# Kernel tuning notes

Hardware: AMD Instinct MI355X
Metric: run time of the kernel (lower is better)

Reference implementation:

```python
import jax, jax.numpy as jnp
import numpy as np

B, N, D, H, FF = 2, 2048, 768, 12, 3072
HD = D // H
RADIUS = 2.0
COORD_DIM = 3
LN_EPS = 1e-5


def _layernorm(x, g, b):
    m = jnp.mean(x, axis=-1, keepdims=True)
    v = jnp.mean((x - m) ** 2, axis=-1, keepdims=True)
    return (x - m) * jax.lax.rsqrt(v + LN_EPS) * g + b


def setup_inputs() -> dict:
    key = jax.random.key(0)
    ks = jax.random.split(key, 16)
    s = 0.02
    return {
        "x": jax.random.normal(ks[0], (B, N, D), jnp.float32),
        "coords": jax.random.uniform(ks[1], (B, N, COORD_DIM), jnp.float32) * 10.0,
        "w_qkv": jax.random.normal(ks[2], (D, 3 * D), jnp.float32) * s,
        "b_qkv": jnp.zeros((3 * D,), jnp.float32),
        "w_out": jax.random.normal(ks[3], (D, D), jnp.float32) * s,
        "b_out": jnp.zeros((D,), jnp.float32),
        "w_ff1": jax.random.normal(ks[4], (D, FF), jnp.float32) * s,
        "b_ff1": jnp.zeros((FF,), jnp.float32),
        "w_ff2": jax.random.normal(ks[5], (FF, D), jnp.float32) * s,
        "b_ff2": jnp.zeros((D,), jnp.float32),
        "g1": jnp.ones((D,), jnp.float32),
        "beta1": jnp.zeros((D,), jnp.float32),
        "g2": jnp.ones((D,), jnp.float32),
        "beta2": jnp.zeros((D,), jnp.float32),
    }


def reference(x, coords, w_qkv, b_qkv, w_out, b_out, w_ff1, b_ff1,
              w_ff2, b_ff2, g1, beta1, g2, beta2):
    # --- attention sub-block ---
    residual = x
    xn = _layernorm(x, g1, beta1)
    qkv = xn @ w_qkv + b_qkv                       # [B,N,3D]
    qkv = qkv.reshape(B, N, 3, H, HD)
    q, k, v = qkv[:, :, 0], qkv[:, :, 1], qkv[:, :, 2]   # [B,N,H,HD]

    # geometric radius mask: attend only to tokens within Euclidean RADIUS
    d2 = jnp.sum((coords[:, :, None, :] - coords[:, None, :, :]) ** 2, axis=-1)  # [B,N,N]
    mask = d2 <= RADIUS * RADIUS                   # self-distance 0 -> always true

    scores = jnp.einsum("bqhd,bkhd->bhqk", q, k) / jnp.sqrt(jnp.float32(HD))
    scores = jnp.where(mask[:, None, :, :], scores, jnp.float32(-1e9))
    attn = jax.nn.softmax(scores, axis=-1)
    attn_out = jnp.einsum("bhqk,bkhd->bqhd", attn, v).reshape(B, N, D)
    attn_out = attn_out @ w_out + b_out            # dropout=0 (eval)
    x = residual + attn_out

    # --- FFN sub-block ---
    residual = x
    xn = _layernorm(x, g2, beta2)
    h = jax.nn.gelu(xn @ w_ff1 + b_ff1, approximate=False)
    ff_out = h @ w_ff2 + b_ff2
    return residual + ff_out
```

## Files before the change

kernel.cpp:

```cpp
#include <hip/hip_runtime.h>
#include <hip/hip_bf16.h>

typedef unsigned short ushort_t;
typedef __attribute__((ext_vector_type(4))) float f32x4;
typedef __attribute__((ext_vector_type(8))) short s16x8;

#define DEV static __device__ __forceinline__

constexpr int Bb = 2, Nn = 2048, Dd = 768, Hh = 12, FFf = 3072;
constexpr int MTOK = Bb * Nn;
constexpr int QKVN = 3 * Dd;

DEV unsigned short f2bf(float f) {
    union { float f; unsigned int i; } x; x.f = f;
    unsigned int r = x.i + 0x7FFFu + ((x.i >> 16) & 1u);
    return (unsigned short)(r >> 16);
}

DEV void gload16(const void* g, void* l) {
    __builtin_amdgcn_global_load_lds(
        (const __attribute__((address_space(1))) void*)g,
        (__attribute__((address_space(3))) void*)l, 16, 0, 0);
}

DEV int xcd_swz(int lin, int n) {
    return (lin & 7) * (n >> 3) + (lin >> 3);
}

DEV float gelu_fast(float x) {
    float u = x * (0.7978845608f + 0.0356774081f * x * x);
    float e = __builtin_amdgcn_exp2f(2.885390082f * u);
    float th = 1.f - 2.f / (e + 1.f);
    return 0.5f * x * (1.f + th);
}

__global__ void k_transpose_all(const float* __restrict__ w_qkv, const float* __restrict__ w_out,
                                const float* __restrict__ w_ff1, const float* __restrict__ w_ff2,
                                unsigned short* __restrict__ o_qkv, unsigned short* __restrict__ o_out,
                                unsigned short* __restrict__ o_ff1, unsigned short* __restrict__ o_ff2) {
    __shared__ float t[32][33];
    int id = blockIdx.x;
    const float* in; unsigned short* out; int K, N, tid;
    if (id < 1728)      { in = w_qkv; out = o_qkv; K = 768;  N = 2304; tid = id; }
    else if (id < 2304) { in = w_out; out = o_out; K = 768;  N = 768;  tid = id - 1728; }
    else if (id < 4608) { in = w_ff1; out = o_ff1; K = 768;  N = 3072; tid = id - 2304; }
    else                { in = w_ff2; out = o_ff2; K = 3072; N = 768;  tid = id - 4608; }
    int nbx = N >> 5;
    int bx = (tid % nbx) * 32, by = (tid / nbx) * 32;
    int tx = threadIdx.x, ty = threadIdx.y;
#pragma unroll
    for (int i = 0; i < 4; i++)
        t[ty + 8 * i][tx] = in[(size_t)(by + ty + 8 * i) * N + bx + tx];
    __syncthreads();
#pragma unroll
    for (int i = 0; i < 4; i++)
        out[(size_t)(bx + ty + 8 * i) * K + by + tx] = f2bf(t[tx][ty + 8 * i]);
}

DEV int cell3(float x, float y, float z) {
    int cx = (int)(x * 0.5f); cx = cx > 4 ? 4 : cx;
    int cy = (int)(y * 0.5f); cy = cy > 4 ? 4 : cy;
    int cz = (int)(z * 0.5f); cz = cz > 4 ? 4 : cz;
    return (cz * 5 + cy) * 5 + cx;
}

__global__ __launch_bounds__(256) void k_sort(const float* __restrict__ coords,
                                              int* __restrict__ s2o,
                                              float4* __restrict__ c4s) {
    int b = blockIdx.y;
    int i = blockIdx.x * 4 + (threadIdx.x >> 6);
    int lane = threadIdx.x & 63;
    const float* cb = coords + (size_t)b * Nn * 3;
    float cix = cb[3 * i], ciy = cb[3 * i + 1], ciz = cb[3 * i + 2];
    int celli = cell3(cix, ciy, ciz);
    int pos = 0;
    for (int it = 0; it < Nn / 64; it++) {
        int j = it * 64 + lane;
        int cj = cell3(cb[3 * j], cb[3 * j + 1], cb[3 * j + 2]);
        bool before = (cj < celli) || (cj == celli && j < i);
        pos += __popcll(__ballot(before));
    }
    if (lane == 0) {
        s2o[b * Nn + pos] = i;
        c4s[b * Nn + pos] = make_float4(cix, ciy, ciz, 0.f);
    }
}

__global__ __launch_bounds__(256) void k_mask(const float4* __restrict__ c4s,
                                              unsigned long long* __restrict__ mb) {
    int qt = blockIdx.x, ks = blockIdx.y, b = blockIdx.z;
    __shared__ float4 ck[256];
    int t = threadIdx.x;
    ck[t] = c4s[b * Nn + ks * 256 + t];
    __syncthreads();
    int r = t >> 2, c = t & 3;
    int q = qt * 64 + r;
    float4 cq = c4s[b * Nn + q];
    unsigned long long w = 0;
#pragma unroll 8
    for (int j = 0; j < 64; j++) {
        float4 k4 = ck[c * 64 + j];
        float dx = __fsub_rn(cq.x, k4.x);
        float dy = __fsub_rn(cq.y, k4.y);
        float dz = __fsub_rn(cq.z, k4.z);
        float d2 = __fadd_rn(__fadd_rn(__fmul_rn(dx, dx), __fmul_rn(dy, dy)),
                             __fmul_rn(dz, dz));
        if (d2 <= 4.0f) w |= 1ull << j;
    }
    mb[((size_t)(b * Nn + q) << 5) + ks * 4 + c] = w;
}

__global__ __launch_bounds__(64) void k_tiles(const unsigned long long* __restrict__ mb,
                                              int* __restrict__ tl) {
    int q64 = blockIdx.x, b = blockIdx.y;
    int lane = threadIdx.x;
    unsigned long long v = 0;
    if (lane < 32) {
        const unsigned long long* base = mb + ((size_t)(b * Nn + q64 * 64) << 5) + lane;
        for (int r = 0; r < 64; r++) v |= base[(size_t)r << 5];
    }
    unsigned long long nz = __ballot(v != 0);
    int idx = __popcll(nz & ((1ull << lane) - 1));
    int* o = tl + (b * 32 + q64) * 33;
    if (v != 0) o[1 + idx] = lane;
    if (lane == 0) o[0] = __popcll(nz);
}

__global__ __launch_bounds__(128) void k_gatherK(const unsigned short* __restrict__ qkv,
                                                 const int* __restrict__ s2o,
                                                 unsigned short* __restrict__ Ksort) {
    int ns = blockIdx.x & (Nn - 1);
    int b = blockIdx.x >> 11;
    int t = threadIdx.x;
    int orig = s2o[b * Nn + ns];
    const s16x8* src = (const s16x8*)(qkv + ((size_t)b * Nn + orig) * QKVN + Dd);
    s16x8* dst = (s16x8*)(Ksort + ((size_t)b * Nn + ns) * Dd);
    if (t < 96) dst[t] = src[t];
}

__global__ __launch_bounds__(256) void k_vt(const unsigned short* __restrict__ qkv,
                                            const int* __restrict__ s2o,
                                            unsigned short* __restrict__ VtT) {
    __shared__ unsigned short Ld[64][72];
    int ns0 = blockIdx.x * 64;
    int bh = blockIdx.y;
    int b = bh / Hh, h = bh % Hh;
    int t = threadIdx.x;
#pragma unroll
    for (int i = 0; i < 2; i++) {
        int item = t + 256 * i;
        int row = item >> 3, ch = (item & 7) * 8;
        int orig = s2o[b * Nn + ns0 + row];
        *(s16x8*)&Ld[row][ch] =
            *(const s16x8*)(qkv + ((size_t)b * Nn + orig) * QKVN + 2 * Dd + h * 64 + ch);
    }
    __syncthreads();
    int vd = (t >> 5) * 8, vkp = (t & 31) * 2;
#pragma unroll
    for (int j = 0; j < 8; j++) {
        unsigned int pack = (unsigned int)Ld[vkp][vd + j] |
                            ((unsigned int)Ld[vkp + 1][vd + j] << 16);
        *(unsigned int*)((char*)VtT +
                         (((size_t)bh * 64 + vd + j) * Nn + ns0 + vkp) * 2) = pack;
    }
}

DEV float wred_sum(float v) {
#pragma unroll
    for (int o = 32; o; o >>= 1) v += __shfl_down(v, o, 64);
    return v;
}

__global__ __launch_bounds__(256) void k_ln(const float* __restrict__ x,
                                            const float* __restrict__ g,
                                            const float* __restrict__ be,
                                            unsigned short* __restrict__ out) {
    int row = blockIdx.x;
    const float* xr = x + (size_t)row * Dd;
    int t = threadIdx.x;
    float v0 = xr[t], v1 = xr[t + 256], v2 = xr[t + 512];
    float s = v0 + v1 + v2;
    float sq = v0 * v0 + v1 * v1 + v2 * v2;
    __shared__ float r1[4], r2[4];
    float ws = wred_sum(s), wq = wred_sum(sq);
    int wid = t >> 6, lane = t & 63;
    if (lane == 0) { r1[wid] = ws; r2[wid] = wq; }
    __syncthreads();
    s = r1[0] + r1[1] + r1[2] + r1[3];
    sq = r2[0] + r2[1] + r2[2] + r2[3];
    float mean = s * (1.f / Dd);
    float var = sq * (1.f / Dd) - mean * mean;
    float rs = rsqrtf(var + 1e-5f);
    unsigned short* orow = out + (size_t)row * Dd;
    orow[t]       = f2bf((v0 - mean) * rs * g[t]       + be[t]);
    orow[t + 256] = f2bf((v1 - mean) * rs * g[t + 256] + be[t + 256]);
    orow[t + 512] = f2bf((v2 - mean) * rs * g[t + 512] + be[t + 512]);
}

#define GEMM_PIPE_LOOP(NT)                                                              \
    stage(0, 0);                                                                        \
    if ((NT) > 1) stage(1, 1);                                                          \
    for (int t = 0; t < (NT); t++) {                                                    \
        int cur = t & 3;                                                                \
        if (t + 2 < (NT)) {                                                             \
            stage((t + 2) & 3, t + 2);                                                  \
            asm volatile("s_waitcnt vmcnt(8)" ::: "memory");                            \
        } else if (t + 1 < (NT)) {                                                      \
            asm volatile("s_waitcnt vmcnt(4)" ::: "memory");                            \
        } else {                                                                        \
            asm volatile("s_waitcnt vmcnt(0)" ::: "memory");                            \
        }                                                                               \
        __builtin_amdgcn_sched_barrier(0);                                              \
        __builtin_amdgcn_s_barrier();                                                   \
        const unsigned short* Ab = As[cur];                                             \
        const unsigned short* Bbp = Bs[cur];                                            \
        s16x8 af[4], bfr[4];                                                            \
        _Pragma("unroll")                                                               \
        for (int i = 0; i < 4; i++) {                                                   \
            af[i]  = *(const s16x8*)&Ab[(wr * 64 + i * 16 + lr) * 32 + lg * 8];         \
            bfr[i] = *(const s16x8*)&Bbp[(wc * 64 + i * 16 + lr) * 32 + lg * 8];        \
        }                                                                               \
        __builtin_amdgcn_s_setprio(1);                                                  \
        _Pragma("unroll")                                                               \
        for (int mi = 0; mi < 4; mi++)                                                  \
            _Pragma("unroll")                                                           \
            for (int ni = 0; ni < 4; ni++)                                              \
                acc[mi][ni] = __builtin_amdgcn_mfma_f32_16x16x32_bf16(                  \
                    af[mi], bfr[ni], acc[mi][ni], 0, 0, 0);                             \
        __builtin_amdgcn_s_setprio(0);                                                  \
    }

template <int EPI>
__global__ __launch_bounds__(256) void k_gemm(const unsigned short* __restrict__ A,
                                              const unsigned short* __restrict__ Bt,
                                              const float* __restrict__ bias,
                                              const float* __restrict__ res,
                                              void* __restrict__ outp,
                                              int M, int N, int K) {
    constexpr int BM = 128, BN = 128, BK = 32;
    __shared__ unsigned short As[4][BM * BK];
    __shared__ unsigned short Bs[4][BN * BK];
    int NB = N >> 7;
    int id = xcd_swz(blockIdx.x, gridDim.x);
    int m0 = (id / NB) * BM, n0 = (id % NB) * BN;
    int t = threadIdx.x;
    int wid = t >> 6, lane = t & 63;
    int wr = wid >> 1, wc = wid & 1;
    int lg = lane >> 4, lr = lane & 15;
    f32x4 acc[4][4] = {};

    int srow = wid * 32 + (lane >> 2);
    int scol = (lane & 3) * 8;
    const unsigned short* Ag = A + (size_t)(m0 + srow) * K + scol;
    const unsigned short* Bg = Bt + (size_t)(n0 + srow) * K + scol;

    auto stage = [&](int buf, int kt) {
        int k0 = kt * BK;
        char* Al = (char*)As[buf] + wid * 2048;
        char* Bl = (char*)Bs[buf] + wid * 2048;
        gload16(Ag + k0, Al);
        gload16(Ag + k0 + (size_t)16 * K, Al + 1024);
        gload16(Bg + k0, Bl);
        gload16(Bg + k0 + (size_t)16 * K, Bl + 1024);
    };
    int nt = K / BK;
    GEMM_PIPE_LOOP(nt)

    int mrow = m0 + wr * 64;
    int ncol = n0 + wc * 64;
#pragma unroll
    for (int mi = 0; mi < 4; mi++) {
#pragma unroll
        for (int ni = 0; ni < 4; ni++) {
            int nn = ncol + ni * 16 + lr;
            float bs = bias[nn];
#pragma unroll
            for (int r = 0; r < 4; r++) {
                int mm = mrow + mi * 16 + lg * 4 + r;
                float v = acc[mi][ni][r] + bs;
                if (EPI == 1) {
                    ((unsigned short*)outp)[(size_t)mm * N + nn] = f2bf(gelu_fast(v));
                } else if (EPI == 2) {
                    v += res[(size_t)mm * N + nn];
                    ((float*)outp)[(size_t)mm * N + nn] = v;
                } else {
                    ((unsigned short*)outp)[(size_t)mm * N + nn] = f2bf(v);
                }
            }
        }
    }
}

template <int SPLIT>
__global__ __launch_bounds__(256) void k_gemm_sk(const unsigned short* __restrict__ A,
                                                 const unsigned short* __restrict__ Bt,
                                                 float* __restrict__ part,
                                                 int M, int N, int K) {
    constexpr int BM = 128, BN = 128, BK = 32;
    __shared__ unsigned short As[4][BM * BK];
    __shared__ unsigned short Bs[4][BN * BK];
    int NB = N >> 7, MB = M >> 7;
    int id = xcd_swz(blockIdx.x, gridDim.x);
    int nb = id % NB;
    int mbk = (id / NB) % MB;
    int kz = id / (NB * MB);
    int m0 = mbk * BM, n0 = nb * BN;
    int Kc = K / SPLIT, kb = kz * (Kc / BK);
    int t = threadIdx.x;
    int wid = t >> 6, lane = t & 63;
    int wr = wid >> 1, wc = wid & 1;
    int lg = lane >> 4, lr = lane & 15;
    f32x4 acc[4][4] = {};

    int srow = wid * 32 + (lane >> 2);
    int scol = (lane & 3) * 8;
    const unsigned short* Ag = A + (size_t)(m0 + srow) * K + scol;
    const unsigned short* Bg = Bt + (size_t)(n0 + srow) * K + scol;

    auto stage = [&](int buf, int kt) {
        int k0 = (kb + kt) * BK;
        char* Al = (char*)As[buf] + wid * 2048;
        char* Bl = (char*)Bs[buf] + wid * 2048;
        gload16(Ag + k0, Al);
        gload16(Ag + k0 + (size_t)16 * K, Al + 1024);
        gload16(Bg + k0, Bl);
        gload16(Bg + k0 + (size_t)16 * K, Bl + 1024);
    };
    int nt = Kc / BK;
    GEMM_PIPE_LOOP(nt)

    float* po = part + (size_t)kz * M * N;
    int mrow = m0 + wr * 64;
    int ncol = n0 + wc * 64;
#pragma unroll
    for (int mi = 0; mi < 4; mi++)
#pragma unroll
        for (int ni = 0; ni < 4; ni++) {
            int nn = ncol + ni * 16 + lr;
#pragma unroll
            for (int r = 0; r < 4; r++) {
                int mm = mrow + mi * 16 + lg * 4 + r;
                po[(size_t)mm * N + nn] = acc[mi][ni][r];
            }
        }
}

__global__ __launch_bounds__(256) void k_reduce2(const float* __restrict__ part,
                                                 const float* __restrict__ bias,
                                                 const float* __restrict__ res,
                                                 float* __restrict__ out,
                                                 int MN, int N) {
    int i = (blockIdx.x * 256 + threadIdx.x) * 4;
    f32x4 a = *(const f32x4*)(part + i);
    f32x4 bq = *(const f32x4*)(part + (size_t)MN + i);
    f32x4 r = *(const f32x4*)(res + i);
    f32x4 bs = *(const f32x4*)(bias + (i % N));
    f32x4 o;
#pragma unroll
    for (int j = 0; j < 4; j++) o[j] = a[j] + bq[j] + bs[j] + r[j];
    *(f32x4*)(out + i) = o;
}

__global__ __launch_bounds__(256) void k_reduce4(const float* __restrict__ part,
                                                 const float* __restrict__ bias,
                                                 const float* __restrict__ res,
                                                 float* __restrict__ out,
                                                 int MN, int N) {
    int i = (blockIdx.x * 256 + threadIdx.x) * 4;
    f32x4 a0 = *(const f32x4*)(part + i);
    f32x4 a1 = *(const f32x4*)(part + (size_t)MN + i);
    f32x4 a2 = *(const f32x4*)(part + 2 * (size_t)MN + i);
    f32x4 a3 = *(const f32x4*)(part + 3 * (size_t)MN + i);
    f32x4 r = *(const f32x4*)(res + i);
    f32x4 bs = *(const f32x4*)(bias + (i % N));
    f32x4 o;
#pragma unroll
    for (int j = 0; j < 4; j++) o[j] = (a0[j] + a1[j]) + (a2[j] + a3[j]) + bs[j] + r[j];
    *(f32x4*)(out + i) = o;
}

constexpr float SC2 = 0.125f * 1.44269504088896340736f;
constexpr float PMASK = -3.0e38f;
constexpr float MINIT = -1.0e30f;

__global__ __launch_bounds__(256) void k_attn(const unsigned short* __restrict__ qkv,
                                              const unsigned short* __restrict__ Ksort,
                                              const unsigned short* __restrict__ VtT,
                                              const int* __restrict__ s2o,
                                              const uint2* __restrict__ mb,
                                              const int* __restrict__ tl,
                                              unsigned short* __restrict__ out) {
    int lin = blockIdx.x;
    int id = (lin & 7) * 96 + (lin >> 3);
    int q64 = id & 31;
    int hb = id >> 5;
    int h = hb % Hh, b = hb / Hh;
    int bh = b * Hh + h;

    __shared__ __align__(16) char sm[2 * 16384 + 4 * 2048];

    int t = threadIdx.x, wid = t >> 6, lane = t & 63;
    int lg = lane >> 4, lr = lane & 15;
    int sw = lr & 7;
    int qbase = q64 * 64 + wid * 16;

    int oq = s2o[b * Nn + qbase + lr];
    const unsigned short* Qb = qkv + ((size_t)b * Nn + oq) * QKVN + h * 64;
    s16x8 qf0 = *(const s16x8*)(Qb + lg * 8);
    s16x8 qf1 = *(const s16x8*)(Qb + 32 + lg * 8);

    const uint2* mrow = mb + ((size_t)(b * Nn + qbase + lr) << 5);
    const int* tle = tl + (b * 32 + q64) * 33;
    int tlv = (lane < 33) ? tle[lane] : 0;
    int cnt = __shfl(tlv, 0, 64);

    int srow = lane >> 3, sch = lane & 7;
    int krow = wid * 8 + srow;
    int kx = sch ^ (krow & 7);
    const unsigned short* Kg0 = Ksort + ((size_t)b * Nn + krow) * Dd + h * 64 + kx * 8;
    const unsigned short* Vg0 = VtT + ((size_t)bh * 64 + krow) * Nn + kx * 8;
    char* pw = sm + 32768 + wid * 2048 + lr * 128;

    float m2 = MINIT, l_run = 0.f;
    f32x4 oacc[4] = {};

    int tid0 = __shfl(tlv, 1, 64);
    uint2 Mw = mrow[tid0];
    {
        char* Kl = sm + wid * 1024;
        gload16(Kg0 + (size_t)(tid0 * 64) * Dd, Kl);
        gload16(Kg0 + (size_t)(tid0 * 64 + 32) * Dd, Kl + 4096);
        char* Vl = sm + 8192 + wid * 1024;
        gload16(Vg0 + tid0 * 64, Vl);
        gload16(Vg0 + tid0 * 64 + 32 * (size_t)Nn, Vl + 4096);
    }
    __syncthreads();

    for (int ti = 0; ti < cnt; ti++) {
        int cur = ti & 1;
        uint2 MwN;
        if (ti + 1 < cnt) {
            int tidn = __shfl(tlv, 2 + ti, 64);
            char* Kl = sm + (cur ^ 1) * 16384 + wid * 1024;
            gload16(Kg0 + (size_t)(tidn * 64) * Dd, Kl);
            gload16(Kg0 + (size_t)(tidn * 64 + 32) * Dd, Kl + 4096);
            char* Vl = sm + (cur ^ 1) * 16384 + 8192 + wid * 1024;
            gload16(Vg0 + tidn * 64, Vl);
            gload16(Vg0 + tidn * 64 + 32 * (size_t)Nn, Vl + 4096);
            MwN = mrow[tidn];
        }

        if (__any((Mw.x | Mw.y) != 0)) {
            const char* Kbuf = sm + cur * 16384;
            const char* Vbuf = Kbuf + 8192;

            __builtin_amdgcn_s_setprio(1);
            f32x4 st[4];
#pragma unroll
            for (int s = 0; s < 4; s++) {
                const char* kr = Kbuf + (s * 16 + lr) * 128;
                s16x8 kf0 = *(const s16x8*)(kr + ((lg ^ sw) << 4));
                s16x8 kf1 = *(const s16x8*)(kr + (((4 + lg) ^ sw) << 4));
                f32x4 z = {};
                z = __builtin_amdgcn_mfma_f32_16x16x32_bf16(kf0, qf0, z, 0, 0, 0);
                st[s] = __builtin_amdgcn_mfma_f32_16x16x32_bf16(kf1, qf1, z, 0, 0, 0);
            }
            __builtin_amdgcn_s_setprio(0);

            float p[4][4];
            float mt = PMASK;
#pragma unroll
            for (int s = 0; s < 4; s++) {
                unsigned int wsel = (s < 2) ? Mw.x : Mw.y;
#pragma unroll
                for (int r = 0; r < 4; r++) {
                    float sv = st[s][r] * SC2;
                    unsigned int bit = (wsel >> ((s & 1) * 16 + lg * 4 + r)) & 1u;
                    p[s][r] = bit ? sv : PMASK;
                    mt = fmaxf(mt, p[s][r]);
                }
            }
            mt = fmaxf(mt, __shfl_xor(mt, 16, 64));
            mt = fmaxf(mt, __shfl_xor(mt, 32, 64));

            if (!__all(mt <= m2 + 11.5416f)) {
                float mn2 = fmaxf(m2, mt);
                float fac = __builtin_amdgcn_exp2f(m2 - mn2);
                l_run *= fac;
                m2 = mn2;
                float fr[4];
#pragma unroll
                for (int r = 0; r < 4; r++) fr[r] = __shfl(fac, (lane & 48) + lg * 4 + r, 64);
#pragma unroll
                for (int dt = 0; dt < 4; dt++)
#pragma unroll
                    for (int r = 0; r < 4; r++) oacc[dt][r] *= fr[r];
            }

            float lt = 0.f;
#pragma unroll
            for (int s = 0; s < 4; s++)
#pragma unroll
                for (int r = 0; r < 4; r++) {
                    p[s][r] = __builtin_amdgcn_exp2f(p[s][r] - m2);
                    lt += p[s][r];
                }
            lt += __shfl_xor(lt, 16, 64);
            lt += __shfl_xor(lt, 32, 64);
            l_run += lt;

#pragma unroll
            for (int s = 0; s < 4; s++) {
                unsigned int lo = (unsigned int)f2bf(p[s][0]) | ((unsigned int)f2bf(p[s][1]) << 16);
                unsigned int hi = (unsigned int)f2bf(p[s][2]) | ((unsigned int)f2bf(p[s][3]) << 16);
                unsigned long long u = (unsigned long long)lo | ((unsigned long long)hi << 32);
                int chunk = (s * 2 + (lg >> 1)) ^ sw;
                *(unsigned long long*)(pw + (chunk << 4) + (lg & 1) * 8) = u;
            }

            __builtin_amdgcn_s_setprio(1);
#pragma unroll
            for (int c = 0; c < 2; c++) {
                s16x8 pf = *(const s16x8*)(pw + (((c * 4 + lg) ^ sw) << 4));
#pragma unroll
                for (int dt = 0; dt < 4; dt++) {
                    const char* vr = Vbuf + (dt * 16 + lr) * 128;
                    s16x8 vf = *(const s16x8*)(vr + (((c * 4 + lg) ^ sw) << 4));
                    oacc[dt] = __builtin_amdgcn_mfma_f32_16x16x32_bf16(pf, vf, oacc[dt], 0, 0, 0);
                }
            }
            __builtin_amdgcn_s_setprio(0);
        }

        __syncthreads();
        Mw = MwN;
    }

    float lr4[4];
    int orow[4];
#pragma unroll
    for (int r = 0; r < 4; r++) {
        lr4[r] = __shfl(l_run, (lane & 48) + lg * 4 + r, 64);
        orow[r] = s2o[b * Nn + qbase + lg * 4 + r];
    }
#pragma unroll
    for (int dt = 0; dt < 4; dt++)
#pragma unroll
        for (int r = 0; r < 4; r++) {
            float v = oacc[dt][r] / lr4[r];
            out[((size_t)b * Nn + orow[r]) * Dd + h * 64 + dt * 16 + lr] = f2bf(v);
        }
}

extern "C" void kernel_launch(void* const* d_in, const int* in_sizes, int n_in,
                              void* d_out, int out_size, void* d_ws, size_t ws_size,
                              hipStream_t stream) {
    const float* x      = (const float*)d_in[0];
    const float* coords = (const float*)d_in[1];
    const float* w_qkv  = (const float*)d_in[2];
    const float* b_qkv  = (const float*)d_in[3];
    const float* w_out  = (const float*)d_in[4];
    const float* b_out  = (const float*)d_in[5];
    const float* w_ff1  = (const float*)d_in[6];
    const float* b_ff1  = (const float*)d_in[7];
    const float* w_ff2  = (const float*)d_in[8];
    const float* b_ff2  = (const float*)d_in[9];
    const float* g1     = (const float*)d_in[10];
    const float* beta1  = (const float*)d_in[11];
    const float* g2     = (const float*)d_in[12];
    const float* beta2  = (const float*)d_in[13];

    char* ws = (char*)d_ws;
    size_t off = 0;
    auto alloc = [&](size_t bytes) {
        char* p = ws + off;
        off += (bytes + 255) & ~(size_t)255;
        return p;
    };
    unsigned short* w_qkv_t = (unsigned short*)alloc((size_t)QKVN * Dd * 2);
    unsigned short* w_out_t = (unsigned short*)alloc((size_t)Dd * Dd * 2);
    unsigned short* w_ff1_t = (unsigned short*)alloc((size_t)FFf * Dd * 2);
    unsigned short* w_ff2_t = (unsigned short*)alloc((size_t)Dd * FFf * 2);
    float4*         c4s     = (float4*)alloc((size_t)MTOK * 16);
    int*            s2o     = (int*)alloc((size_t)MTOK * 4);
    unsigned long long* mbits = (unsigned long long*)alloc((size_t)MTOK * 32 * 8);
    int*            tl      = (int*)alloc((size_t)Bb * 32 * 33 * 4);
    unsigned short* xn      = (unsigned short*)alloc((size_t)MTOK * Dd * 2);
    unsigned short* hbuf    = (unsigned short*)alloc((size_t)MTOK * FFf * 2);
    float*          x2      = (float*)alloc((size_t)MTOK * Dd * 4);
    unsigned short* attn_o  = (unsigned short*)alloc((size_t)MTOK * Dd * 2);
    unsigned short* qkv     = (unsigned short*)alloc((size_t)MTOK * QKVN * 2);
    unsigned short* Ksort   = (unsigned short*)alloc((size_t)MTOK * Dd * 2);
    unsigned short* VtT     = (unsigned short*)alloc((size_t)Bb * Hh * 64 * Nn * 2);
    float*          partial = (float*)alloc((size_t)4 * MTOK * Dd * 4);

    k_transpose_all<<<dim3(6912), dim3(32, 8), 0, stream>>>(
        w_qkv, w_out, w_ff1, w_ff2, w_qkv_t, w_out_t, w_ff1_t, w_ff2_t);
    k_sort<<<dim3(Nn / 4, Bb), 256, 0, stream>>>(coords, s2o, c4s);
    k_mask<<<dim3(Nn / 64, 8, Bb), 256, 0, stream>>>(c4s, mbits);
    k_tiles<<<dim3(32, Bb), 64, 0, stream>>>(mbits, tl);

    k_ln<<<MTOK, 256, 0, stream>>>(x, g1, beta1, xn);
    k_gemm<0><<<dim3((QKVN / 128) * (MTOK / 128)), 256, 0, stream>>>(
        xn, w_qkv_t, b_qkv, nullptr, qkv, MTOK, QKVN, Dd);
    k_gatherK<<<dim3(MTOK), 128, 0, stream>>>(qkv, s2o, Ksort);
    k_vt<<<dim3(Nn / 64, Bb * Hh), 256, 0, stream>>>(qkv, s2o, VtT);
    k_attn<<<dim3((Nn / 64) * Hh * Bb), 256, 0, stream>>>(
        qkv, Ksort, VtT, s2o, (const uint2*)mbits, tl, attn_o);
    k_gemm_sk<2><<<dim3((Dd / 128) * (MTOK / 128) * 2), 256, 0, stream>>>(
        attn_o, w_out_t, partial, MTOK, Dd, Dd);
    k_reduce2<<<dim3(MTOK * Dd / 1024), 256, 0, stream>>>(
        partial, b_out, x, x2, MTOK * Dd, Dd);
    k_ln<<<MTOK, 256, 0, stream>>>(x2, g2, beta2, xn);
    k_gemm<1><<<dim3((FFf / 128) * (MTOK / 128)), 256, 0, stream>>>(
        xn, w_ff1_t, b_ff1, nullptr, hbuf, MTOK, FFf, Dd);
    k_gemm_sk<4><<<dim3((Dd / 128) * (MTOK / 128) * 4), 256, 0, stream>>>(
        hbuf, w_ff2_t, partial, MTOK, Dd, FFf);
    k_reduce4<<<dim3(MTOK * Dd / 1024), 256, 0, stream>>>(
        partial, b_ff2, x2, (float*)d_out, MTOK * Dd, Dd);
}
```

Baseline: 224.1 us.

## Shrink GEMM tiles to 128x64 with double buffering and fuse reduce with LayerNorm

The GEMM kernels now use 128x64 output tiles instead of 128x128, with a two-stage LDS pipeline instead of four stages. This doubles the block count and cuts LDS use, which should raise occupancy on the 256-CU device. In exchange there is less data reuse per tile and a second barrier per k-step. Separately, the split-K reduce for the attention output projection is fused with the second LayerNorm (one wave per row), removing one kernel launch and one full read of x2.

```diff
diff --git a/kernel.cpp b/kernel.cpp
--- a/kernel.cpp
+++ b/kernel.cpp
@@ -199,14 +199,11 @@
 
 #define GEMM_PIPE_LOOP(NT)                                                              \
     stage(0, 0);                                                                        \
-    if ((NT) > 1) stage(1, 1);                                                          \
     for (int t = 0; t < (NT); t++) {                                                    \
-        int cur = t & 3;                                                                \
-        if (t + 2 < (NT)) {                                                             \
-            stage((t + 2) & 3, t + 2);                                                  \
-            asm volatile("s_waitcnt vmcnt(8)" ::: "memory");                            \
-        } else if (t + 1 < (NT)) {                                                      \
-            asm volatile("s_waitcnt vmcnt(4)" ::: "memory");                            \
+        int cur = t & 1;                                                                \
+        if (t + 1 < (NT)) {                                                             \
+            stage(cur ^ 1, t + 1);                                                      \
+            asm volatile("s_waitcnt vmcnt(3)" ::: "memory");                            \
         } else {                                                                        \
             asm volatile("s_waitcnt vmcnt(0)" ::: "memory");                            \
         }                                                                               \
@@ -214,20 +211,22 @@
         __builtin_amdgcn_s_barrier();                                                   \
         const unsigned short* Ab = As[cur];                                             \
         const unsigned short* Bbp = Bs[cur];                                            \
-        s16x8 af[4], bfr[4];                                                            \
+        s16x8 af[4], bfr[2];                                                            \
         _Pragma("unroll")                                                               \
-        for (int i = 0; i < 4; i++) {                                                   \
-            af[i]  = *(const s16x8*)&Ab[(wr * 64 + i * 16 + lr) * 32 + lg * 8];         \
-            bfr[i] = *(const s16x8*)&Bbp[(wc * 64 + i * 16 + lr) * 32 + lg * 8];        \
-        }                                                                               \
+        for (int i = 0; i < 4; i++)                                                     \
+            af[i] = *(const s16x8*)&Ab[(wr * 64 + i * 16 + lr) * 32 + lg * 8];          \
+        _Pragma("unroll")                                                               \
+        for (int i = 0; i < 2; i++)                                                     \
+            bfr[i] = *(const s16x8*)&Bbp[(wc * 32 + i * 16 + lr) * 32 + lg * 8];        \
         __builtin_amdgcn_s_setprio(1);                                                  \
         _Pragma("unroll")                                                               \
         for (int mi = 0; mi < 4; mi++)                                                  \
             _Pragma("unroll")                                                           \
-            for (int ni = 0; ni < 4; ni++)                                              \
+            for (int ni = 0; ni < 2; ni++)                                              \
                 acc[mi][ni] = __builtin_amdgcn_mfma_f32_16x16x32_bf16(                  \
                     af[mi], bfr[ni], acc[mi][ni], 0, 0, 0);                             \
         __builtin_amdgcn_s_setprio(0);                                                  \
+        __builtin_amdgcn_s_barrier();                                                   \
     }
 
 template <int EPI>
@@ -237,41 +236,40 @@
                                               const float* __restrict__ res,
                                               void* __restrict__ outp,
                                               int M, int N, int K) {
-    constexpr int BM = 128, BN = 128, BK = 32;
-    __shared__ unsigned short As[4][BM * BK];
-    __shared__ unsigned short Bs[4][BN * BK];
-    int NB = N >> 7;
+    constexpr int BM = 128, BN = 64, BK = 32;
+    __shared__ unsigned short As[2][BM * BK];
+    __shared__ unsigned short Bs[2][BN * BK];
+    int NB = N >> 6;
     int id = xcd_swz(blockIdx.x, gridDim.x);
     int m0 = (id / NB) * BM, n0 = (id % NB) * BN;
     int t = threadIdx.x;
     int wid = t >> 6, lane = t & 63;
     int wr = wid >> 1, wc = wid & 1;
     int lg = lane >> 4, lr = lane & 15;
-    f32x4 acc[4][4] = {};
-
-    int srow = wid * 32 + (lane >> 2);
+    f32x4 acc[4][2] = {};
+
+    int sr = lane >> 2;
     int scol = (lane & 3) * 8;
-    const unsigned short* Ag = A + (size_t)(m0 + srow) * K + scol;
-    const unsigned short* Bg = Bt + (size_t)(n0 + srow) * K + scol;
+    const unsigned short* Ag = A + (size_t)(m0 + wid * 32 + sr) * K + scol;
+    const unsigned short* Bg = Bt + (size_t)(n0 + wid * 16 + sr) * K + scol;
 
     auto stage = [&](int buf, int kt) {
         int k0 = kt * BK;
         char* Al = (char*)As[buf] + wid * 2048;
-        char* Bl = (char*)Bs[buf] + wid * 2048;
+        char* Bl = (char*)Bs[buf] + wid * 1024;
         gload16(Ag + k0, Al);
         gload16(Ag + k0 + (size_t)16 * K, Al + 1024);
         gload16(Bg + k0, Bl);
-        gload16(Bg + k0 + (size_t)16 * K, Bl + 1024);
     };
     int nt = K / BK;
     GEMM_PIPE_LOOP(nt)
 
     int mrow = m0 + wr * 64;
-    int ncol = n0 + wc * 64;
+    int ncol = n0 + wc * 32;
 #pragma unroll
     for (int mi = 0; mi < 4; mi++) {
 #pragma unroll
-        for (int ni = 0; ni < 4; ni++) {
+        for (int ni = 0; ni < 2; ni++) {
             int nn = ncol + ni * 16 + lr;
             float bs = bias[nn];
 #pragma unroll
@@ -296,10 +294,10 @@
                                                  const unsigned short* __restrict__ Bt,
                                                  float* __restrict__ part,
                                                  int M, int N, int K) {
-    constexpr int BM = 128, BN = 128, BK = 32;
-    __shared__ unsigned short As[4][BM * BK];
-    __shared__ unsigned short Bs[4][BN * BK];
-    int NB = N >> 7, MB = M >> 7;
+    constexpr int BM = 128, BN = 64, BK = 32;
+    __shared__ unsigned short As[2][BM * BK];
+    __shared__ unsigned short Bs[2][BN * BK];
+    int NB = N >> 6, MB = M >> 7;
     int id = xcd_swz(blockIdx.x, gridDim.x);
     int nb = id % NB;
     int mbk = (id / NB) % MB;
@@ -310,32 +308,31 @@
     int wid = t >> 6, lane = t & 63;
     int wr = wid >> 1, wc = wid & 1;
     int lg = lane >> 4, lr = lane & 15;
-    f32x4 acc[4][4] = {};
-
-    int srow = wid * 32 + (lane >> 2);
+    f32x4 acc[4][2] = {};
+
+    int sr = lane >> 2;
     int scol = (lane & 3) * 8;
-    const unsigned short* Ag = A + (size_t)(m0 + srow) * K + scol;
-    const unsigned short* Bg = Bt + (size_t)(n0 + srow) * K + scol;
+    const unsigned short* Ag = A + (size_t)(m0 + wid * 32 + sr) * K + scol;
+    const unsigned short* Bg = Bt + (size_t)(n0 + wid * 16 + sr) * K + scol;
 
     auto stage = [&](int buf, int kt) {
         int k0 = (kb + kt) * BK;
         char* Al = (char*)As[buf] + wid * 2048;
-        char* Bl = (char*)Bs[buf] + wid * 2048;
+        char* Bl = (char*)Bs[buf] + wid * 1024;
         gload16(Ag + k0, Al);
         gload16(Ag + k0 + (size_t)16 * K, Al + 1024);
         gload16(Bg + k0, Bl);
-        gload16(Bg + k0 + (size_t)16 * K, Bl + 1024);
     };
     int nt = Kc / BK;
     GEMM_PIPE_LOOP(nt)
 
     float* po = part + (size_t)kz * M * N;
     int mrow = m0 + wr * 64;
-    int ncol = n0 + wc * 64;
+    int ncol = n0 + wc * 32;
 #pragma unroll
     for (int mi = 0; mi < 4; mi++)
 #pragma unroll
-        for (int ni = 0; ni < 4; ni++) {
+        for (int ni = 0; ni < 2; ni++) {
             int nn = ncol + ni * 16 + lr;
 #pragma unroll
             for (int r = 0; r < 4; r++) {
@@ -345,20 +342,51 @@
         }
 }
 
-__global__ __launch_bounds__(256) void k_reduce2(const float* __restrict__ part,
-                                                 const float* __restrict__ bias,
-                                                 const float* __restrict__ res,
-                                                 float* __restrict__ out,
-                                                 int MN, int N) {
-    int i = (blockIdx.x * 256 + threadIdx.x) * 4;
-    f32x4 a = *(const f32x4*)(part + i);
-    f32x4 bq = *(const f32x4*)(part + (size_t)MN + i);
-    f32x4 r = *(const f32x4*)(res + i);
-    f32x4 bs = *(const f32x4*)(bias + (i % N));
-    f32x4 o;
-#pragma unroll
-    for (int j = 0; j < 4; j++) o[j] = a[j] + bq[j] + bs[j] + r[j];
-    *(f32x4*)(out + i) = o;
+__global__ __launch_bounds__(256) void k_reduce2_ln(const float* __restrict__ part,
+                                                    const float* __restrict__ bias,
+                                                    const float* __restrict__ res,
+                                                    const float* __restrict__ g,
+                                                    const float* __restrict__ be,
+                                                    float* __restrict__ x2,
+                                                    unsigned short* __restrict__ xn,
+                                                    int MN) {
+    int wid = threadIdx.x >> 6, lane = threadIdx.x & 63;
+    int row = blockIdx.x * 4 + wid;
+    size_t base = (size_t)row * Dd;
+    f32x4 v[3];
+    float s = 0.f, sq = 0.f;
+#pragma unroll
+    for (int j = 0; j < 3; j++) {
+        int col = j * 256 + lane * 4;
+        f32x4 a = *(const f32x4*)(part + base + col);
+        f32x4 b = *(const f32x4*)(part + (size_t)MN + base + col);
+        f32x4 r = *(const f32x4*)(res + base + col);
+        f32x4 bs = *(const f32x4*)(bias + col);
+#pragma unroll
+        for (int q = 0; q < 4; q++) {
+            v[j][q] = a[q] + b[q] + bs[q] + r[q];
+            s += v[j][q];
+            sq += v[j][q] * v[j][q];
+        }
+        *(f32x4*)(x2 + base + col) = v[j];
+    }
+    s = wred_sum(s); sq = wred_sum(sq);
+    s = __shfl(s, 0, 64); sq = __shfl(sq, 0, 64);
+    float mean = s * (1.f / Dd);
+    float var = sq * (1.f / Dd) - mean * mean;
+    float rs = rsqrtf(var + 1e-5f);
+#pragma unroll
+    for (int j = 0; j < 3; j++) {
+        int col = j * 256 + lane * 4;
+        f32x4 gg = *(const f32x4*)(g + col);
+        f32x4 bb = *(const f32x4*)(be + col);
+        ushort4 o;
+        o.x = f2bf((v[j][0] - mean) * rs * gg[0] + bb[0]);
+        o.y = f2bf((v[j][1] - mean) * rs * gg[1] + bb[1]);
+        o.z = f2bf((v[j][2] - mean) * rs * gg[2] + bb[2]);
+        o.w = f2bf((v[j][3] - mean) * rs * gg[3] + bb[3]);
+        *(ushort4*)(xn + base + col) = o;
+    }
 }
 
 __global__ __launch_bounds__(256) void k_reduce4(const float* __restrict__ part,
@@ -601,20 +629,19 @@
     k_tiles<<<dim3(32, Bb), 64, 0, stream>>>(mbits, tl);
 
     k_ln<<<MTOK, 256, 0, stream>>>(x, g1, beta1, xn);
-    k_gemm<0><<<dim3((QKVN / 128) * (MTOK / 128)), 256, 0, stream>>>(
+    k_gemm<0><<<dim3((QKVN / 64) * (MTOK / 128)), 256, 0, stream>>>(
         xn, w_qkv_t, b_qkv, nullptr, qkv, MTOK, QKVN, Dd);
     k_gatherK<<<dim3(MTOK), 128, 0, stream>>>(qkv, s2o, Ksort);
     k_vt<<<dim3(Nn / 64, Bb * Hh), 256, 0, stream>>>(qkv, s2o, VtT);
     k_attn<<<dim3((Nn / 64) * Hh * Bb), 256, 0, stream>>>(
         qkv, Ksort, VtT, s2o, (const uint2*)mbits, tl, attn_o);
-    k_gemm_sk<2><<<dim3((Dd / 128) * (MTOK / 128) * 2), 256, 0, stream>>>(
+    k_gemm_sk<2><<<dim3((Dd / 64) * (MTOK / 128) * 2), 256, 0, stream>>>(
         attn_o, w_out_t, partial, MTOK, Dd, Dd);
-    k_reduce2<<<dim3(MTOK * Dd / 1024), 256, 0, stream>>>(
-        partial, b_out, x, x2, MTOK * Dd, Dd);
-    k_ln<<<MTOK, 256, 0, stream>>>(x2, g2, beta2, xn);
-    k_gemm<1><<<dim3((FFf / 128) * (MTOK / 128)), 256, 0, stream>>>(
+    k_reduce2_ln<<<dim3(MTOK / 4), 256, 0, stream>>>(
+        partial, b_out, x, g2, beta2, x2, xn, MTOK * Dd);
+    k_gemm<1><<<dim3((FFf / 64) * (MTOK / 128)), 256, 0, stream>>>(
         xn, w_ff1_t, b_ff1, nullptr, hbuf, MTOK, FFf, Dd);
-    k_gemm_sk<4><<<dim3((Dd / 128) * (MTOK / 128) * 4), 256, 0, stream>>>(
+    k_gemm_sk<4><<<dim3((Dd / 64) * (MTOK / 128) * 4), 256, 0, stream>>>(
         hbuf, w_ff2_t, partial, MTOK, Dd, FFf);
     k_reduce4<<<dim3(MTOK * Dd / 1024), 256, 0, stream>>>(
         partial, b_ff2, x2, (float*)d_out, MTOK * Dd, Dd);
```

After: 231.7 us. 3.4% more time.
